# Performance work log

Hardware: AMD Instinct MI355X
Metric: run time of the kernel (lower is better)

Reference implementation:

```python
import jax, jax.numpy as jnp
import numpy as np

N = 100000
SK = [10, 5]
LN_EPS = 1e-5


def setup_inputs() -> dict:
    key = jax.random.key(0)
    ks = jax.random.split(key, 12)
    F_IN, H, OUT = 256, 128, 64
    X = jax.random.normal(ks[0], (N, F_IN), dtype=jnp.float32)
    edge_index = jax.random.randint(ks[1], (2, 1600000), 0, N, dtype=jnp.int64)
    # cached sampled-neighbor index lists: cumulative fanout 10, then 10*5=50 per node
    sn0 = jax.random.randint(ks[2], (N * SK[0],), 0, N, dtype=jnp.int64)
    sn1 = jax.random.randint(ks[3], (N * SK[0] * SK[1],), 0, N, dtype=jnp.int64)
    s1 = 1.0 / np.sqrt(F_IN)
    s2 = 1.0 / np.sqrt(2 * H)
    s3 = 1.0 / np.sqrt(H)
    W1 = jax.random.uniform(ks[4], (F_IN, H), jnp.float32, -s1, s1)
    b1 = jax.random.uniform(ks[5], (H,), jnp.float32, -s1, s1)
    W2 = jax.random.uniform(ks[6], (2 * H, H), jnp.float32, -s2, s2)
    b2 = jax.random.uniform(ks[7], (H,), jnp.float32, -s2, s2)
    gamma = jnp.ones((H,), jnp.float32)
    beta = jnp.zeros((H,), jnp.float32)
    W3 = jax.random.uniform(ks[8], (H, OUT), jnp.float32, -s3, s3)
    b3 = jax.random.uniform(ks[9], (OUT,), jnp.float32, -s3, s3)
    return {"X": X, "edge_index": edge_index, "sn0": sn0, "sn1": sn1,
            "W1": W1, "b1": b1, "W2": W2, "b2": b2,
            "gamma": gamma, "beta": beta, "W3": W3, "b3": b3}


def _layernorm(x, gamma, beta):
    mu = jnp.mean(x, axis=-1, keepdims=True)
    var = jnp.mean(jnp.square(x - mu), axis=-1, keepdims=True)
    return (x - mu) * jax.lax.rsqrt(var + LN_EPS) * gamma + beta


def reference(X, edge_index, sn0, sn1, W1, b1, W2, b2, gamma, beta, W3, b3):
    # edge_index is only used in the original to build the cached adjacency
    # used for sampling; sampled indices (sn0, sn1) are precomputed inputs.
    del edge_index
    h = X @ W1 + b1  # [N, H]
    num_update = 1
    for sn, k in ((sn0, SK[0]), (sn1, SK[1])):
        num_update *= k
        # neighbor gather + sum reduce: [N*num_update, H] -> [N, num_update, H] -> [N, H]
        agg = h[sn].reshape(N, num_update, -1).sum(axis=1)
        h = jnp.concatenate([h, agg], axis=1) @ W2 + b2  # concat agg_hidden
        h = _layernorm(jax.nn.relu(h), gamma, beta)
    return h @ W3 + b3
```

## Files before the change

kernel.cpp:

```cpp
#include <hip/hip_runtime.h>


typedef unsigned short u16;
typedef unsigned int   u32;

#define NN  100000
#define NT  6250
#define HID 128
#define FIN 256

typedef __attribute__((ext_vector_type(8))) short bf16x8;
typedef __attribute__((ext_vector_type(4))) float f32x4;

__device__ __forceinline__ u16 f2bf(float f) {
  u32 x = __builtin_bit_cast(u32, f);
  x += 0x7fffu + ((x >> 16) & 1u);
  return (u16)(x >> 16);
}
__device__ __forceinline__ float bflo(u32 v) { return __builtin_bit_cast(float, v << 16); }
__device__ __forceinline__ float bfhi(u32 v) { return __builtin_bit_cast(float, v & 0xffff0000u); }

__global__ __launch_bounds__(256) void prep_kernel(
    const float* __restrict__ W1, const float* __restrict__ W2, const float* __restrict__ W3,
    u16* __restrict__ W1T, u16* __restrict__ W2T, u16* __restrict__ W3T) {
  int t = blockIdx.x * 256 + threadIdx.x;
  if (t < FIN * HID) {
    int k = t >> 7, c = t & (HID - 1);
    W1T[c * FIN + k] = f2bf(W1[t]);
    W2T[c * FIN + k] = f2bf(W2[t]);
  }
  if (t < HID * 64) {
    int k = t >> 6, c = t & 63;
    W3T[c * HID + k] = f2bf(W3[t]);
  }
}

__global__ __launch_bounds__(256) void proj_kernel(
    const float* __restrict__ X, const float* __restrict__ b1,
    const u16* __restrict__ W1T, u16* __restrict__ h1) {
  const int w = threadIdx.x >> 6, l = threadIdx.x & 63;
  const int tile = blockIdx.x * 4 + w;
  if (tile >= NT) return;
  const int lr = l & 15, lg = l >> 4;

  bf16x8 a[8];
  const float* xb = X + (tile * 16 + lr) * FIN + lg * 8;
  #pragma unroll
  for (int s = 0; s < 8; ++s) {
    const float4* p = (const float4*)(xb + s * 32);
    float4 x0 = p[0], x1 = p[1];
    bf16x8 t;
    t[0] = (short)f2bf(x0.x); t[1] = (short)f2bf(x0.y);
    t[2] = (short)f2bf(x0.z); t[3] = (short)f2bf(x0.w);
    t[4] = (short)f2bf(x1.x); t[5] = (short)f2bf(x1.y);
    t[6] = (short)f2bf(x1.z); t[7] = (short)f2bf(x1.w);
    a[s] = t;
  }
  #pragma unroll
  for (int n = 0; n < 8; ++n) {
    const int col = n * 16 + lr;
    f32x4 c = {0.f, 0.f, 0.f, 0.f};
    const bf16x8* wp = (const bf16x8*)(W1T + col * FIN + lg * 8);
    #pragma unroll
    for (int s = 0; s < 8; ++s)
      c = __builtin_amdgcn_mfma_f32_16x16x32_bf16(a[s], wp[s * 4], c, 0, 0, 0);
    const float bias = b1[col];
    #pragma unroll
    for (int r = 0; r < 4; ++r)
      h1[(tile * 16 + lg * 4 + r) * HID + col] = f2bf(c[r] + bias);
  }
}

template <int KN>
__global__ __launch_bounds__(256, 6) void gather_kernel(
    const u16* __restrict__ h, const int* __restrict__ sn, u16* __restrict__ agg) {
  const int wid = (int)((blockIdx.x * 256u + threadIdx.x) >> 6);
  if (wid >= NN) return;
  const int node = __builtin_amdgcn_readfirstlane(wid);
  const int l = threadIdx.x & 63;
  const u16* hp = h + 2 * l;
  const int* sp = sn + (size_t)node * KN;
  float a0 = 0.f, a1 = 0.f;
  #pragma unroll
  for (int j = 0; j < KN; ++j) {
    const int idx = sp[j];
    const u32 v = *(const u32*)(hp + (size_t)idx * HID);
    a0 += bflo(v); a1 += bfhi(v);
  }
  *(u32*)(agg + (size_t)node * HID + 2 * l) = ((u32)f2bf(a1) << 16) | (u32)f2bf(a0);
}

template <bool FINAL>
__global__ __launch_bounds__(512, 4) void mlp_kernel(
    const u16* __restrict__ hin, const u16* __restrict__ aggin,
    const u16* __restrict__ W2T, const float* __restrict__ b2,
    const float* __restrict__ gamma, const float* __restrict__ beta,
    const u16* __restrict__ W3T, const float* __restrict__ b3,
    u16* __restrict__ hout, float* __restrict__ out) {
  const int w = threadIdx.x >> 6, l = threadIdx.x & 63;
  const int lr = l & 15, lg = l >> 4;
  const int tile = blockIdx.x * 8 + w;
  const bool active = tile < NT;

  f32x4 acc[8];
  if (active) {
    const int row = tile * 16 + lr;
    bf16x8 a[8];
    const u16* hb = hin  + (size_t)row * HID + lg * 8;
    const u16* ab = aggin + (size_t)row * HID + lg * 8;
    #pragma unroll
    for (int s = 0; s < 4; ++s) a[s]     = *(const bf16x8*)(hb + s * 32);
    #pragma unroll
    for (int s = 0; s < 4; ++s) a[4 + s] = *(const bf16x8*)(ab + s * 32);

    #pragma unroll
    for (int n = 0; n < 8; ++n) {
      f32x4 c = {0.f, 0.f, 0.f, 0.f};
      const bf16x8* wp = (const bf16x8*)(W2T + (n * 16 + lr) * FIN + lg * 8);
      #pragma unroll
      for (int s = 0; s < 8; ++s)
        c = __builtin_amdgcn_mfma_f32_16x16x32_bf16(a[s], wp[s * 4], c, 0, 0, 0);
      acc[n] = c;
    }
    #pragma unroll
    for (int n = 0; n < 8; ++n) {
      const float bias = b2[n * 16 + lr];
      #pragma unroll
      for (int r = 0; r < 4; ++r) {
        const float v = acc[n][r] + bias;
        acc[n][r] = v > 0.f ? v : 0.f;
      }
    }
    #pragma unroll
    for (int r = 0; r < 4; ++r) {
      float s1 = 0.f, s2 = 0.f;
      #pragma unroll
      for (int n = 0; n < 8; ++n) { const float v = acc[n][r]; s1 += v; s2 += v * v; }
      s1 += __shfl_xor(s1, 1); s2 += __shfl_xor(s2, 1);
      s1 += __shfl_xor(s1, 2); s2 += __shfl_xor(s2, 2);
      s1 += __shfl_xor(s1, 4); s2 += __shfl_xor(s2, 4);
      s1 += __shfl_xor(s1, 8); s2 += __shfl_xor(s2, 8);
      const float mu  = s1 * (1.f / 128.f);
      const float var = s2 * (1.f / 128.f) - mu * mu;
      const float rstd = rsqrtf(var + 1e-5f);
      #pragma unroll
      for (int n = 0; n < 8; ++n)
        acc[n][r] = (acc[n][r] - mu) * rstd;
    }
  }

  if constexpr (!FINAL) {
    if (active) {
      #pragma unroll
      for (int n = 0; n < 8; ++n) {
        const int col = n * 16 + lr;
        const float g = gamma[col], bb = beta[col];
        #pragma unroll
        for (int r = 0; r < 4; ++r)
          hout[(size_t)(tile * 16 + lg * 4 + r) * HID + col] = f2bf(acc[n][r] * g + bb);
      }
    }
  } else {
    __shared__ u16 At[8][16][264];
    if (active) {
      #pragma unroll
      for (int n = 0; n < 8; ++n) {
        const int col = n * 16 + lr;
        const float g = gamma[col], bb = beta[col];
        #pragma unroll
        for (int r = 0; r < 4; ++r)
          At[w][lg * 4 + r][col] = f2bf(acc[n][r] * g + bb);
      }
    }
    __syncthreads();
    if (active) {
      bf16x8 a2[4];
      #pragma unroll
      for (int s = 0; s < 4; ++s)
        a2[s] = *(const bf16x8*)&At[w][lr][s * 32 + lg * 8];
      #pragma unroll
      for (int n = 0; n < 4; ++n) {
        f32x4 c = {0.f, 0.f, 0.f, 0.f};
        const bf16x8* wp = (const bf16x8*)(W3T + (n * 16 + lr) * HID + lg * 8);
        #pragma unroll
        for (int s = 0; s < 4; ++s)
          c = __builtin_amdgcn_mfma_f32_16x16x32_bf16(a2[s], wp[s * 4], c, 0, 0, 0);
        const int col = n * 16 + lr;
        const float bias = b3[col];
        #pragma unroll
        for (int r = 0; r < 4; ++r)
          out[(size_t)(tile * 16 + lg * 4 + r) * 64 + col] = c[r] + bias;
      }
    }
  }
}

extern "C" void kernel_launch(void* const* d_in, const int* in_sizes, int n_in,
                              void* d_out, int out_size, void* d_ws, size_t ws_size,
                              hipStream_t stream) {
  (void)in_sizes; (void)n_in; (void)out_size; (void)ws_size;
  const float* X   = (const float*)d_in[0];
  const int*   sn0 = (const int*)d_in[2];
  const int*   sn1 = (const int*)d_in[3];
  const float* W1  = (const float*)d_in[4];
  const float* b1  = (const float*)d_in[5];
  const float* W2  = (const float*)d_in[6];
  const float* b2  = (const float*)d_in[7];
  const float* gm  = (const float*)d_in[8];
  const float* bt  = (const float*)d_in[9];
  const float* W3  = (const float*)d_in[10];
  const float* b3  = (const float*)d_in[11];
  float* out = (float*)d_out;

  char* ws = (char*)d_ws;
  u16* slotA = (u16*)(ws);
  u16* slotB = (u16*)(ws + 25600000);
  u16* W1T = (u16*)(ws + 51200000);
  u16* W2T = (u16*)(ws + 51265536);
  u16* W3T = (u16*)(ws + 51331072);

  u16* h1 = slotA;
  u16* agg1 = slotB;
  u16* h2 = slotB;
  u16* agg2 = slotA;

  prep_kernel<<<128, 256, 0, stream>>>(W1, W2, W3, W1T, W2T, W3T);
  proj_kernel<<<(NT + 3) / 4, 256, 0, stream>>>(X, b1, W1T, h1);
  gather_kernel<10><<<NN / 4, 256, 0, stream>>>(h1, sn0, agg1);
  mlp_kernel<false><<<(NT + 7) / 8, 512, 0, stream>>>(
      h1, agg1, W2T, b2, gm, bt, nullptr, nullptr, h2, nullptr);
  gather_kernel<50><<<NN / 4, 256, 0, stream>>>(h2, sn1, agg2);
  mlp_kernel<true><<<(NT + 7) / 8, 512, 0, stream>>>(
      h2, agg2, W2T, b2, gm, bt, W3T, b3, nullptr, out);
}
```

Baseline: 577.7 us.

## Split hidden activations into two 64-column planes and gather each plane separately

Hidden states and aggregates are stored as two separate 64-column bf16 planes instead of one 128-column row-major array. Each neighbor-gather pass now launches twice, once per plane, so each pass works over a table half the size, which is meant to improve cache hit rates on the random row gathers. The MLP kernels read and write the split planes. The cost is reading the neighbor index arrays twice, narrower 2-byte per-lane loads, and two extra kernel launches.

```diff
diff --git a/kernel.cpp b/kernel.cpp
--- a/kernel.cpp
+++ b/kernel.cpp
@@ -8,6 +8,7 @@
 #define NT  6250
 #define HID 128
 #define FIN 256
+#define NPL 64
 
 typedef __attribute__((ext_vector_type(8))) short bf16x8;
 typedef __attribute__((ext_vector_type(4))) float f32x4;
@@ -17,8 +18,9 @@
   x += 0x7fffu + ((x >> 16) & 1u);
   return (u16)(x >> 16);
 }
-__device__ __forceinline__ float bflo(u32 v) { return __builtin_bit_cast(float, v << 16); }
-__device__ __forceinline__ float bfhi(u32 v) { return __builtin_bit_cast(float, v & 0xffff0000u); }
+__device__ __forceinline__ float bf2f(u16 v) {
+  return __builtin_bit_cast(float, (u32)v << 16);
+}
 
 __global__ __launch_bounds__(256) void prep_kernel(
     const float* __restrict__ W1, const float* __restrict__ W2, const float* __restrict__ W3,
@@ -37,14 +39,14 @@
 
 __global__ __launch_bounds__(256) void proj_kernel(
     const float* __restrict__ X, const float* __restrict__ b1,
-    const u16* __restrict__ W1T, u16* __restrict__ h1) {
+    const u16* __restrict__ W1T, u16* __restrict__ h1lo, u16* __restrict__ h1hi) {
   const int w = threadIdx.x >> 6, l = threadIdx.x & 63;
   const int tile = blockIdx.x * 4 + w;
   if (tile >= NT) return;
   const int lr = l & 15, lg = l >> 4;
 
   bf16x8 a[8];
-  const float* xb = X + (tile * 16 + lr) * FIN + lg * 8;
+  const float* xb = X + (size_t)(tile * 16 + lr) * FIN + lg * 8;
   #pragma unroll
   for (int s = 0; s < 8; ++s) {
     const float4* p = (const float4*)(xb + s * 32);
@@ -65,38 +67,40 @@
     for (int s = 0; s < 8; ++s)
       c = __builtin_amdgcn_mfma_f32_16x16x32_bf16(a[s], wp[s * 4], c, 0, 0, 0);
     const float bias = b1[col];
+    u16* dst = (n < 4) ? h1lo : h1hi;
+    const int pc = (n & 3) * 16 + lr;
     #pragma unroll
     for (int r = 0; r < 4; ++r)
-      h1[(tile * 16 + lg * 4 + r) * HID + col] = f2bf(c[r] + bias);
+      dst[(size_t)(tile * 16 + lg * 4 + r) * NPL + pc] = f2bf(c[r] + bias);
   }
 }
 
 template <int KN>
-__global__ __launch_bounds__(256, 6) void gather_kernel(
-    const u16* __restrict__ h, const int* __restrict__ sn, u16* __restrict__ agg) {
+__global__ __launch_bounds__(256) void gather_kernel(
+    const u16* __restrict__ hp_, const int* __restrict__ sn, u16* __restrict__ aggp) {
   const int wid = (int)((blockIdx.x * 256u + threadIdx.x) >> 6);
   if (wid >= NN) return;
   const int node = __builtin_amdgcn_readfirstlane(wid);
   const int l = threadIdx.x & 63;
-  const u16* hp = h + 2 * l;
+  const u16* hp = hp_ + l;
   const int* sp = sn + (size_t)node * KN;
-  float a0 = 0.f, a1 = 0.f;
+  float a0 = 0.f;
   #pragma unroll
   for (int j = 0; j < KN; ++j) {
     const int idx = sp[j];
-    const u32 v = *(const u32*)(hp + (size_t)idx * HID);
-    a0 += bflo(v); a1 += bfhi(v);
-  }
-  *(u32*)(agg + (size_t)node * HID + 2 * l) = ((u32)f2bf(a1) << 16) | (u32)f2bf(a0);
+    a0 += bf2f(hp[(size_t)idx * NPL]);
+  }
+  aggp[(size_t)node * NPL + l] = f2bf(a0);
 }
 
 template <bool FINAL>
 __global__ __launch_bounds__(512, 4) void mlp_kernel(
-    const u16* __restrict__ hin, const u16* __restrict__ aggin,
+    const u16* __restrict__ hinlo, const u16* __restrict__ hinhi,
+    const u16* agglo, const u16* agghi,
     const u16* __restrict__ W2T, const float* __restrict__ b2,
     const float* __restrict__ gamma, const float* __restrict__ beta,
     const u16* __restrict__ W3T, const float* __restrict__ b3,
-    u16* __restrict__ hout, float* __restrict__ out) {
+    u16* houtlo, u16* houthi, float* __restrict__ out) {
   const int w = threadIdx.x >> 6, l = threadIdx.x & 63;
   const int lr = l & 15, lg = l >> 4;
   const int tile = blockIdx.x * 8 + w;
@@ -104,14 +108,20 @@
 
   f32x4 acc[8];
   if (active) {
-    const int row = tile * 16 + lr;
+    const size_t row = (size_t)(tile * 16 + lr);
     bf16x8 a[8];
-    const u16* hb = hin  + (size_t)row * HID + lg * 8;
-    const u16* ab = aggin + (size_t)row * HID + lg * 8;
-    #pragma unroll
-    for (int s = 0; s < 4; ++s) a[s]     = *(const bf16x8*)(hb + s * 32);
-    #pragma unroll
-    for (int s = 0; s < 4; ++s) a[4 + s] = *(const bf16x8*)(ab + s * 32);
+    const u16* hlo = hinlo + row * NPL + lg * 8;
+    const u16* hhi = hinhi + row * NPL + lg * 8;
+    const u16* alo = agglo + row * NPL + lg * 8;
+    const u16* ahi = agghi + row * NPL + lg * 8;
+    a[0] = *(const bf16x8*)(hlo);
+    a[1] = *(const bf16x8*)(hlo + 32);
+    a[2] = *(const bf16x8*)(hhi);
+    a[3] = *(const bf16x8*)(hhi + 32);
+    a[4] = *(const bf16x8*)(alo);
+    a[5] = *(const bf16x8*)(alo + 32);
+    a[6] = *(const bf16x8*)(ahi);
+    a[7] = *(const bf16x8*)(ahi + 32);
 
     #pragma unroll
     for (int n = 0; n < 8; ++n) {
@@ -155,9 +165,11 @@
       for (int n = 0; n < 8; ++n) {
         const int col = n * 16 + lr;
         const float g = gamma[col], bb = beta[col];
+        u16* dst = (n < 4) ? houtlo : houthi;
+        const int pc = (n & 3) * 16 + lr;
         #pragma unroll
         for (int r = 0; r < 4; ++r)
-          hout[(size_t)(tile * 16 + lg * 4 + r) * HID + col] = f2bf(acc[n][r] * g + bb);
+          dst[(size_t)(tile * 16 + lg * 4 + r) * NPL + pc] = f2bf(acc[n][r] * g + bb);
       }
     }
   } else {
@@ -212,24 +224,24 @@
   const float* b3  = (const float*)d_in[11];
   float* out = (float*)d_out;
 
+  const size_t PL = (size_t)NN * NPL * sizeof(u16);
   char* ws = (char*)d_ws;
-  u16* slotA = (u16*)(ws);
-  u16* slotB = (u16*)(ws + 25600000);
-  u16* W1T = (u16*)(ws + 51200000);
-  u16* W2T = (u16*)(ws + 51265536);
-  u16* W3T = (u16*)(ws + 51331072);
-
-  u16* h1 = slotA;
-  u16* agg1 = slotB;
-  u16* h2 = slotB;
-  u16* agg2 = slotA;
+  u16* A0 = (u16*)(ws);
+  u16* A1 = (u16*)(ws + PL);
+  u16* B0 = (u16*)(ws + 2 * PL);
+  u16* B1 = (u16*)(ws + 3 * PL);
+  u16* W1T = (u16*)(ws + 4 * PL);
+  u16* W2T = (u16*)(ws + 4 * PL + 65536);
+  u16* W3T = (u16*)(ws + 4 * PL + 131072);
 
   prep_kernel<<<128, 256, 0, stream>>>(W1, W2, W3, W1T, W2T, W3T);
-  proj_kernel<<<(NT + 3) / 4, 256, 0, stream>>>(X, b1, W1T, h1);
-  gather_kernel<10><<<NN / 4, 256, 0, stream>>>(h1, sn0, agg1);
+  proj_kernel<<<(NT + 3) / 4, 256, 0, stream>>>(X, b1, W1T, A0, A1);
+  gather_kernel<10><<<NN / 4, 256, 0, stream>>>(A0, sn0, B0);
+  gather_kernel<10><<<NN / 4, 256, 0, stream>>>(A1, sn0, B1);
   mlp_kernel<false><<<(NT + 7) / 8, 512, 0, stream>>>(
-      h1, agg1, W2T, b2, gm, bt, nullptr, nullptr, h2, nullptr);
-  gather_kernel<50><<<NN / 4, 256, 0, stream>>>(h2, sn1, agg2);
+      A0, A1, B0, B1, W2T, b2, gm, bt, nullptr, nullptr, B0, B1, nullptr);
+  gather_kernel<50><<<NN / 4, 256, 0, stream>>>(B0, sn1, A0);
+  gather_kernel<50><<<NN / 4, 256, 0, stream>>>(B1, sn1, A1);
   mlp_kernel<true><<<(NT + 7) / 8, 512, 0, stream>>>(
-      h2, agg2, W2T, b2, gm, bt, W3T, b3, nullptr, out);
-}
+      B0, B1, A0, A1, W2T, b2, gm, bt, W3T, b3, nullptr, nullptr, out);
+}
```

Measured after the change: 549.4 us. -4.9%, faster.
